# Kernel tuning notes

Measured on AMD Instinct MI355X. Metric: run time of the kernel, lower is better.

The kernel has to match this reference:

```python
import jax, jax.numpy as jnp
import numpy as np

B, M, N, DQ, H = 4, 4096, 4096, 256, 64

def setup_inputs() -> dict:
    key = jax.random.key(0)
    k1, k2, k3, k4 = jax.random.split(key, 4)
    x = jax.random.normal(k1, (B, M, DQ), dtype=jnp.float32)
    cond = jax.random.normal(k2, (B, N, DQ), dtype=jnp.float32)
    Wq = jax.random.normal(k3, (DQ, H), dtype=jnp.float32) * (1.0 / np.sqrt(DQ))
    Wkv = jax.random.normal(k4, (DQ, 2 * H), dtype=jnp.float32) * (1.0 / np.sqrt(DQ))
    return {"x": x, "cond": cond, "Wq": Wq, "Wkv": Wkv}

def reference(x, cond, Wq, Wkv):
    h = Wq.shape[1]
    q = jnp.einsum('bmi,ih->bmh', x, Wq)          # [B,M,H]
    kv = jnp.einsum('bni,ih->bnh', cond, Wkv)     # [B,N,2H]
    k, v = jnp.split(kv, 2, axis=-1)              # each [B,N,H]
    qk = jnp.einsum('bmd,bnd->bmn', q, k) / jnp.sqrt(jnp.asarray(h, q.dtype))
    attn = jax.nn.softmax(qk, axis=-1)            # [B,M,N]
    out = jnp.einsum('bmn,bnd->bmd', attn, v)     # [B,M,H]
    return out
```

## Files before the change

kernel.cpp:

```cpp
#include <hip/hip_runtime.h>
#include <hip/hip_bf16.h>
#include <cstdint>


#define BB 4
#define MM 4096
#define NN 4096
#define DQm 256
#define DH 64
#define NSP 4
#define QSCALE 0.18033688011112042f

typedef _Float16 half8 __attribute__((ext_vector_type(8)));
typedef _Float16 half4 __attribute__((ext_vector_type(4)));
typedef float floatx16 __attribute__((ext_vector_type(16)));

static __device__ __forceinline__ unsigned pkrtz(float a, float b) {
    union { __fp16 h __attribute__((ext_vector_type(2))); unsigned u; } cv;
    cv.h = __builtin_amdgcn_cvt_pkrtz(a, b);
    return cv.u;
}

__global__ __launch_bounds__(256) void wtrans_kernel(const float* __restrict__ Wq,
                                                     const float* __restrict__ Wkv,
                                                     _Float16* __restrict__ wt) {
    int cout = blockIdx.x;
    int t = threadIdx.x;
    float v = (cout < 64) ? Wq[t * 64 + cout] * QSCALE : Wkv[t * 128 + (cout - 64)];
    _Float16 hi = (_Float16)v;
    _Float16 lo = (_Float16)(v - (float)hi);
    wt[cout * DQm + t] = hi;
    wt[192 * DQm + cout * DQm + t] = lo;
}

__global__ __launch_bounds__(256) void qproj_kernel(const float* __restrict__ x,
                                                    const _Float16* __restrict__ wt,
                                                    _Float16* __restrict__ q_h) {
    __shared__ __align__(16) _Float16 xh[64][264];
    __shared__ __align__(16) _Float16 xl[64][264];
    const int t = threadIdx.x;
    const long row0 = (long)blockIdx.x * 64;
    const float4* xg = (const float4*)(x + row0 * DQm);
#pragma unroll
    for (int it = 0; it < 16; ++it) {
        int fid = t + it * 256;
        int row = fid >> 6, c4 = fid & 63;
        float4 v = xg[fid];
        half4 hh = {(_Float16)v.x, (_Float16)v.y, (_Float16)v.z, (_Float16)v.w};
        half4 hl = {(_Float16)(v.x - (float)hh[0]), (_Float16)(v.y - (float)hh[1]),
                    (_Float16)(v.z - (float)hh[2]), (_Float16)(v.w - (float)hh[3])};
        *(half4*)(&xh[row][c4 * 4]) = hh;
        *(half4*)(&xl[row][c4 * 4]) = hl;
    }
    __syncthreads();
    const int lane = t & 63, w = t >> 6, c = lane & 31, h = lane >> 5;
    const int rt = w & 1, ct = w >> 1;
    const _Float16* wlo = wt + 192 * DQm;
    floatx16 a1, a2, a3;
#pragma unroll
    for (int i = 0; i < 16; ++i) { a1[i] = 0.f; a2[i] = 0.f; a3[i] = 0.f; }
#pragma unroll
    for (int kt = 0; kt < 16; ++kt) {
        half8 ah = *(const half8*)(&xh[rt * 32 + c][kt * 16 + h * 8]);
        half8 al = *(const half8*)(&xl[rt * 32 + c][kt * 16 + h * 8]);
        half8 bh = *(const half8*)(wt  + (long)(ct * 32 + c) * DQm + kt * 16 + h * 8);
        half8 bl = *(const half8*)(wlo + (long)(ct * 32 + c) * DQm + kt * 16 + h * 8);
        a1 = __builtin_amdgcn_mfma_f32_32x32x16_f16(ah, bh, a1, 0, 0, 0);
        a2 = __builtin_amdgcn_mfma_f32_32x32x16_f16(ah, bl, a2, 0, 0, 0);
        a3 = __builtin_amdgcn_mfma_f32_32x32x16_f16(al, bh, a3, 0, 0, 0);
    }
#pragma unroll
    for (int r = 0; r < 16; ++r) {
        int m = (r & 3) + 8 * (r >> 2) + 4 * h;
        q_h[(row0 + rt * 32 + m) * DH + ct * 32 + c] = (_Float16)(a1[r] + a2[r] + a3[r]);
    }
}

__global__ __launch_bounds__(256) void kvproj_kernel(const float* __restrict__ cond,
                                                     const _Float16* __restrict__ wt,
                                                     _Float16* __restrict__ k_h,
                                                     _Float16* __restrict__ vt_h) {
    __shared__ __align__(16) _Float16 xh[64][264];
    __shared__ __align__(16) _Float16 xl[64][264];
    const int t = threadIdx.x;
    const long row0 = (long)blockIdx.x * 64;
    const float4* xg = (const float4*)(cond + row0 * DQm);
#pragma unroll
    for (int it = 0; it < 16; ++it) {
        int fid = t + it * 256;
        int row = fid >> 6, c4 = fid & 63;
        float4 v = xg[fid];
        half4 hh = {(_Float16)v.x, (_Float16)v.y, (_Float16)v.z, (_Float16)v.w};
        half4 hl = {(_Float16)(v.x - (float)hh[0]), (_Float16)(v.y - (float)hh[1]),
                    (_Float16)(v.z - (float)hh[2]), (_Float16)(v.w - (float)hh[3])};
        *(half4*)(&xh[row][c4 * 4]) = hh;
        *(half4*)(&xl[row][c4 * 4]) = hl;
    }
    __syncthreads();
    const int lane = t & 63, w = t >> 6, c = lane & 31, h = lane >> 5;
    const int rt = w & 1, ctp = w >> 1;
    const _Float16* wlo = wt + 192 * DQm;
    floatx16 a1[2], a2[2], a3[2];
#pragma unroll
    for (int i = 0; i < 16; ++i) {
        a1[0][i] = 0.f; a2[0][i] = 0.f; a3[0][i] = 0.f;
        a1[1][i] = 0.f; a2[1][i] = 0.f; a3[1][i] = 0.f;
    }
#pragma unroll
    for (int kt = 0; kt < 16; ++kt) {
        half8 ah = *(const half8*)(&xh[rt * 32 + c][kt * 16 + h * 8]);
        half8 al = *(const half8*)(&xl[rt * 32 + c][kt * 16 + h * 8]);
#pragma unroll
        for (int i = 0; i < 2; ++i) {
            long wrow = 64 + (ctp * 2 + i) * 32 + c;
            half8 bh = *(const half8*)(wt  + wrow * DQm + kt * 16 + h * 8);
            half8 bl = *(const half8*)(wlo + wrow * DQm + kt * 16 + h * 8);
            a1[i] = __builtin_amdgcn_mfma_f32_32x32x16_f16(ah, bh, a1[i], 0, 0, 0);
            a2[i] = __builtin_amdgcn_mfma_f32_32x32x16_f16(ah, bl, a2[i], 0, 0, 0);
            a3[i] = __builtin_amdgcn_mfma_f32_32x32x16_f16(al, bh, a3[i], 0, 0, 0);
        }
    }
#pragma unroll
    for (int i = 0; i < 2; ++i) {
        int cout = (ctp * 2 + i) * 32 + c;
        if (cout < 64) {
#pragma unroll
            for (int r = 0; r < 16; ++r) {
                int m = (r & 3) + 8 * (r >> 2) + 4 * h;
                k_h[(row0 + rt * 32 + m) * DH + cout] =
                    (_Float16)(a1[i][r] + a2[i][r] + a3[i][r]);
            }
        } else {
            int d = cout - 64;
            long bb = row0 >> 12;
#pragma unroll
            for (int s2 = 0; s2 < 4; ++s2) {
                long n = row0 + rt * 32 + 8 * s2 + 4 * h;
                half4 hv;
#pragma unroll
                for (int j = 0; j < 4; ++j)
                    hv[j] = (_Float16)(a1[i][s2 * 4 + j] + a2[i][s2 * 4 + j] +
                                       a3[i][s2 * 4 + j]);
                *(half4*)(vt_h + (bb * DH + d) * NN + (n & 4095)) = hv;
            }
        }
    }
}

__global__ __launch_bounds__(256, 2) void fa_kernel(const _Float16* __restrict__ q_h,
                                                    const _Float16* __restrict__ k_h,
                                                    const _Float16* __restrict__ vt_h,
                                                    float* __restrict__ Opart,
                                                    float2* __restrict__ ml) {
    __shared__ __align__(16) _Float16 k_lds[64][72];
    __shared__ __align__(16) _Float16 vt_lds[64][72];

    const int t = threadIdx.x;
    const int w = t >> 6;
    const int lane = t & 63;
    const int c = lane & 31;
    const int h = lane >> 5;

    const int bid = blockIdx.x;
    const int sp = bid >> 7;
    const int b  = (bid >> 5) & 3;
    const int mt = bid & 31;
    const int mbase = mt * 128 + w * 32;
    const long qrow = (long)b * MM + mbase + c;

    half8 qf[4];
#pragma unroll
    for (int kt = 0; kt < 4; ++kt)
        qf[kt] = *(const half8*)(q_h + qrow * DH + kt * 16 + h * 8);

    floatx16 Oc0, Oc1;
#pragma unroll
    for (int i = 0; i < 16; ++i) { Oc0[i] = 0.f; Oc1[i] = 0.f; }
    float m_run = -INFINITY, l_run = 0.f;

#pragma unroll 1
    for (int nt = sp * 16; nt < sp * 16 + 16; ++nt) {
        const int n0 = nt * 64;
        __syncthreads();
        {
            const uint4* kg = (const uint4*)(k_h + ((long)b * NN + n0) * DH);
#pragma unroll
            for (int it = 0; it < 2; ++it) {
                int cid = t + it * 256;
                int r = cid >> 3, q = cid & 7;
                *(uint4*)(&k_lds[r][q * 8]) = kg[cid];
                *(uint4*)(&vt_lds[r][q * 8]) =
                    *(const uint4*)(vt_h + ((long)b * DH + r) * NN + n0 + q * 8);
            }
        }
        __syncthreads();

        floatx16 Sc[2];
#pragma unroll
        for (int a = 0; a < 2; ++a) {
            floatx16 acc;
#pragma unroll
            for (int i = 0; i < 16; ++i) acc[i] = 0.f;
#pragma unroll
            for (int kt = 0; kt < 4; ++kt) {
                half8 af = *(const half8*)(&k_lds[a * 32 + c][kt * 16 + h * 8]);
                acc = __builtin_amdgcn_mfma_f32_32x32x16_f16(af, qf[kt], acc, 0, 0, 0);
            }
            Sc[a] = acc;
        }

        float tmax = -INFINITY;
#pragma unroll
        for (int a = 0; a < 2; ++a)
#pragma unroll
            for (int r = 0; r < 16; ++r) tmax = fmaxf(tmax, Sc[a][r]);
        tmax = fmaxf(tmax, __shfl_xor(tmax, 32, 64));
        float m_new = fmaxf(m_run, tmax);
        float alpha = exp2f(m_run - m_new);
        float tsum = 0.f;
#pragma unroll
        for (int a = 0; a < 2; ++a)
#pragma unroll
            for (int r = 0; r < 16; ++r) {
                float p = exp2f(Sc[a][r] - m_new);
                Sc[a][r] = p;
                tsum += p;
            }
        tsum += __shfl_xor(tsum, 32, 64);
        l_run = l_run * alpha + tsum;
        m_run = m_new;
#pragma unroll
        for (int i = 0; i < 16; ++i) { Oc0[i] *= alpha; Oc1[i] *= alpha; }

#pragma unroll
        for (int a = 0; a < 2; ++a) {
            uint2 pk0 = {pkrtz(Sc[a][0],  Sc[a][1]),  pkrtz(Sc[a][2],  Sc[a][3])};
            uint2 pk1 = {pkrtz(Sc[a][4],  Sc[a][5]),  pkrtz(Sc[a][6],  Sc[a][7])};
            uint2 pk2 = {pkrtz(Sc[a][8],  Sc[a][9]),  pkrtz(Sc[a][10], Sc[a][11])};
            uint2 pk3 = {pkrtz(Sc[a][12], Sc[a][13]), pkrtz(Sc[a][14], Sc[a][15])};
            uint2 s0, s1, ex0, ex1;
            s0.x = h ? pk0.x : pk1.x;  s0.y = h ? pk0.y : pk1.y;
            s1.x = h ? pk2.x : pk3.x;  s1.y = h ? pk2.y : pk3.y;
            ex0.x = __shfl_xor((int)s0.x, 32, 64);
            ex0.y = __shfl_xor((int)s0.y, 32, 64);
            ex1.x = __shfl_xor((int)s1.x, 32, 64);
            ex1.y = __shfl_xor((int)s1.y, 32, 64);
            union { uint4 u; half8 f; } f0, f1;
            f0.u.x = h ? ex0.x : pk0.x;  f0.u.y = h ? ex0.y : pk0.y;
            f0.u.z = h ? pk1.x : ex0.x;  f0.u.w = h ? pk1.y : ex0.y;
            f1.u.x = h ? ex1.x : pk2.x;  f1.u.y = h ? ex1.y : pk2.y;
            f1.u.z = h ? pk3.x : ex1.x;  f1.u.w = h ? pk3.y : ex1.y;
#pragma unroll
            for (int bq = 0; bq < 2; ++bq) {
                int kt = 2 * a + bq;
                half8 pf = bq ? f1.f : f0.f;
                half8 vf0 = *(const half8*)(&vt_lds[c][kt * 16 + h * 8]);
                half8 vf1 = *(const half8*)(&vt_lds[32 + c][kt * 16 + h * 8]);
                Oc0 = __builtin_amdgcn_mfma_f32_32x32x16_f16(vf0, pf, Oc0, 0, 0, 0);
                Oc1 = __builtin_amdgcn_mfma_f32_32x32x16_f16(vf1, pf, Oc1, 0, 0, 0);
            }
        }
    }

    const long obase = ((long)sp * BB * MM + (long)b * MM + mbase + c) * DH;
#pragma unroll
    for (int dt = 0; dt < 2; ++dt) {
        const floatx16& O = dt ? Oc1 : Oc0;
#pragma unroll
        for (int s2 = 0; s2 < 4; ++s2) {
            float4 v;
            v.x = O[s2 * 4 + 0]; v.y = O[s2 * 4 + 1];
            v.z = O[s2 * 4 + 2]; v.w = O[s2 * 4 + 3];
            *(float4*)(Opart + obase + dt * 32 + s2 * 8 + h * 4) = v;
        }
    }
    if (h == 0)
        ml[((long)sp * BB + b) * MM + mbase + c] = make_float2(m_run, l_run);
}

__global__ __launch_bounds__(256) void merge_kernel(const float* __restrict__ Opart,
                                                    const float2* __restrict__ ml,
                                                    float* __restrict__ out) {
    const long gid = (long)blockIdx.x * 256 + threadIdx.x;
    const long row = gid >> 6;
    float2 p[NSP];
    float mmax = -INFINITY;
#pragma unroll
    for (int i = 0; i < NSP; ++i) {
        p[i] = ml[(long)i * BB * MM + row];
        mmax = fmaxf(mmax, p[i].x);
    }
    float denom = 0.f, o = 0.f;
#pragma unroll
    for (int i = 0; i < NSP; ++i) {
        float ai = exp2f(p[i].x - mmax);
        denom += ai * p[i].y;
        o += ai * Opart[(long)i * BB * MM * DH + gid];
    }
    out[gid] = o / denom;
}

extern "C" void kernel_launch(void* const* d_in, const int* in_sizes, int n_in,
                              void* d_out, int out_size, void* d_ws, size_t ws_size,
                              hipStream_t stream) {
    const float* x    = (const float*)d_in[0];
    const float* cond = (const float*)d_in[1];
    const float* Wq   = (const float*)d_in[2];
    const float* Wkv  = (const float*)d_in[3];
    float* out = (float*)d_out;

    char* ws = (char*)d_ws;
    _Float16* wt   = (_Float16*)(ws);
    _Float16* q_h  = (_Float16*)(ws + 196608);
    _Float16* k_h  = (_Float16*)(ws + 196608 + 2097152);
    _Float16* vt_h = (_Float16*)(ws + 196608 + 2 * 2097152);
    float*    Op   = (float*)(ws + 196608 + 3 * 2097152);
    float2*   mlp  = (float2*)(ws + 196608 + 3 * 2097152 + (size_t)NSP * 4194304);

    wtrans_kernel<<<192, 256, 0, stream>>>(Wq, Wkv, wt);
    qproj_kernel<<<BB * MM / 64, 256, 0, stream>>>(x, wt, q_h);
    kvproj_kernel<<<BB * NN / 64, 256, 0, stream>>>(cond, wt, k_h, vt_h);
    fa_kernel<<<NSP * BB * 32, 256, 0, stream>>>(q_h, k_h, vt_h, Op, mlp);
    merge_kernel<<<BB * MM * DH / 256, 256, 0, stream>>>(Op, mlp, out);
}
```

Before: 138.2 us.

## Merge projection kernels, double split-K, lazy softmax rescale, permlane32 swap

Fuses the Q and KV projection kernels into one launch so both run concurrently. Doubles the number of key-dimension splits in the attention kernel and raises the launch-bounds occupancy hint from 2 to 4 blocks per CU, giving more blocks and shorter loops. The online softmax now rescales the running max and accumulators only when some lane's new max exceeds the old one by more than 8 (log2 domain). P fragments are exchanged with permlane32_swap instead of shuffles. The trade-offs are more partial outputs for the merge kernel to combine, tighter register limits, and a bounded range for unnormalised exponentials.

Measured after the change: 134.9 us. 2.4% less time.

```diff
diff --git a/kernel.cpp b/kernel.cpp
--- a/kernel.cpp
+++ b/kernel.cpp
@@ -8,7 +8,8 @@
 #define NN 4096
 #define DQm 256
 #define DH 64
-#define NSP 4
+#define NSP 8
+#define NITER (NN / 64 / NSP)
 #define QSCALE 0.18033688011112042f
 
 typedef _Float16 half8 __attribute__((ext_vector_type(8)));
@@ -33,14 +34,19 @@
     wt[192 * DQm + cout * DQm + t] = lo;
 }
 
-__global__ __launch_bounds__(256) void qproj_kernel(const float* __restrict__ x,
-                                                    const _Float16* __restrict__ wt,
-                                                    _Float16* __restrict__ q_h) {
+__global__ __launch_bounds__(256) void proj_kernel(const float* __restrict__ x,
+                                                   const float* __restrict__ cond,
+                                                   const _Float16* __restrict__ wt,
+                                                   _Float16* __restrict__ q_h,
+                                                   _Float16* __restrict__ k_h,
+                                                   _Float16* __restrict__ vt_h) {
     __shared__ __align__(16) _Float16 xh[64][264];
     __shared__ __align__(16) _Float16 xl[64][264];
     const int t = threadIdx.x;
-    const long row0 = (long)blockIdx.x * 64;
-    const float4* xg = (const float4*)(x + row0 * DQm);
+    const bool isq = blockIdx.x < (BB * MM / 64);
+    const int blk = isq ? blockIdx.x : blockIdx.x - BB * MM / 64;
+    const long row0 = (long)blk * 64;
+    const float4* xg = (const float4*)((isq ? x : cond) + row0 * DQm);
 #pragma unroll
     for (int it = 0; it < 16; ++it) {
         int fid = t + it * 256;
@@ -54,100 +60,79 @@
     }
     __syncthreads();
     const int lane = t & 63, w = t >> 6, c = lane & 31, h = lane >> 5;
-    const int rt = w & 1, ct = w >> 1;
     const _Float16* wlo = wt + 192 * DQm;
-    floatx16 a1, a2, a3;
-#pragma unroll
-    for (int i = 0; i < 16; ++i) { a1[i] = 0.f; a2[i] = 0.f; a3[i] = 0.f; }
-#pragma unroll
-    for (int kt = 0; kt < 16; ++kt) {
-        half8 ah = *(const half8*)(&xh[rt * 32 + c][kt * 16 + h * 8]);
-        half8 al = *(const half8*)(&xl[rt * 32 + c][kt * 16 + h * 8]);
-        half8 bh = *(const half8*)(wt  + (long)(ct * 32 + c) * DQm + kt * 16 + h * 8);
-        half8 bl = *(const half8*)(wlo + (long)(ct * 32 + c) * DQm + kt * 16 + h * 8);
-        a1 = __builtin_amdgcn_mfma_f32_32x32x16_f16(ah, bh, a1, 0, 0, 0);
-        a2 = __builtin_amdgcn_mfma_f32_32x32x16_f16(ah, bl, a2, 0, 0, 0);
-        a3 = __builtin_amdgcn_mfma_f32_32x32x16_f16(al, bh, a3, 0, 0, 0);
-    }
-#pragma unroll
-    for (int r = 0; r < 16; ++r) {
-        int m = (r & 3) + 8 * (r >> 2) + 4 * h;
-        q_h[(row0 + rt * 32 + m) * DH + ct * 32 + c] = (_Float16)(a1[r] + a2[r] + a3[r]);
-    }
-}
-
-__global__ __launch_bounds__(256) void kvproj_kernel(const float* __restrict__ cond,
-                                                     const _Float16* __restrict__ wt,
-                                                     _Float16* __restrict__ k_h,
-                                                     _Float16* __restrict__ vt_h) {
-    __shared__ __align__(16) _Float16 xh[64][264];
-    __shared__ __align__(16) _Float16 xl[64][264];
-    const int t = threadIdx.x;
-    const long row0 = (long)blockIdx.x * 64;
-    const float4* xg = (const float4*)(cond + row0 * DQm);
-#pragma unroll
-    for (int it = 0; it < 16; ++it) {
-        int fid = t + it * 256;
-        int row = fid >> 6, c4 = fid & 63;
-        float4 v = xg[fid];
-        half4 hh = {(_Float16)v.x, (_Float16)v.y, (_Float16)v.z, (_Float16)v.w};
-        half4 hl = {(_Float16)(v.x - (float)hh[0]), (_Float16)(v.y - (float)hh[1]),
-                    (_Float16)(v.z - (float)hh[2]), (_Float16)(v.w - (float)hh[3])};
-        *(half4*)(&xh[row][c4 * 4]) = hh;
-        *(half4*)(&xl[row][c4 * 4]) = hl;
-    }
-    __syncthreads();
-    const int lane = t & 63, w = t >> 6, c = lane & 31, h = lane >> 5;
-    const int rt = w & 1, ctp = w >> 1;
-    const _Float16* wlo = wt + 192 * DQm;
-    floatx16 a1[2], a2[2], a3[2];
-#pragma unroll
-    for (int i = 0; i < 16; ++i) {
-        a1[0][i] = 0.f; a2[0][i] = 0.f; a3[0][i] = 0.f;
-        a1[1][i] = 0.f; a2[1][i] = 0.f; a3[1][i] = 0.f;
-    }
-#pragma unroll
-    for (int kt = 0; kt < 16; ++kt) {
-        half8 ah = *(const half8*)(&xh[rt * 32 + c][kt * 16 + h * 8]);
-        half8 al = *(const half8*)(&xl[rt * 32 + c][kt * 16 + h * 8]);
+
+    if (isq) {
+        const int rt = w & 1, ct = w >> 1;
+        floatx16 a1, a2, a3;
+#pragma unroll
+        for (int i = 0; i < 16; ++i) { a1[i] = 0.f; a2[i] = 0.f; a3[i] = 0.f; }
+#pragma unroll
+        for (int kt = 0; kt < 16; ++kt) {
+            half8 ah = *(const half8*)(&xh[rt * 32 + c][kt * 16 + h * 8]);
+            half8 al = *(const half8*)(&xl[rt * 32 + c][kt * 16 + h * 8]);
+            half8 bh = *(const half8*)(wt  + (long)(ct * 32 + c) * DQm + kt * 16 + h * 8);
+            half8 bl = *(const half8*)(wlo + (long)(ct * 32 + c) * DQm + kt * 16 + h * 8);
+            a1 = __builtin_amdgcn_mfma_f32_32x32x16_f16(ah, bh, a1, 0, 0, 0);
+            a2 = __builtin_amdgcn_mfma_f32_32x32x16_f16(ah, bl, a2, 0, 0, 0);
+            a3 = __builtin_amdgcn_mfma_f32_32x32x16_f16(al, bh, a3, 0, 0, 0);
+        }
+#pragma unroll
+        for (int r = 0; r < 16; ++r) {
+            int m = (r & 3) + 8 * (r >> 2) + 4 * h;
+            q_h[(row0 + rt * 32 + m) * DH + ct * 32 + c] = (_Float16)(a1[r] + a2[r] + a3[r]);
+        }
+    } else {
+        const int rt = w & 1, ctp = w >> 1;
+        floatx16 a1[2], a2[2], a3[2];
+#pragma unroll
+        for (int i = 0; i < 16; ++i) {
+            a1[0][i] = 0.f; a2[0][i] = 0.f; a3[0][i] = 0.f;
+            a1[1][i] = 0.f; a2[1][i] = 0.f; a3[1][i] = 0.f;
+        }
+#pragma unroll
+        for (int kt = 0; kt < 16; ++kt) {
+            half8 ah = *(const half8*)(&xh[rt * 32 + c][kt * 16 + h * 8]);
+            half8 al = *(const half8*)(&xl[rt * 32 + c][kt * 16 + h * 8]);
+#pragma unroll
+            for (int i = 0; i < 2; ++i) {
+                long wrow = 64 + (ctp * 2 + i) * 32 + c;
+                half8 bh = *(const half8*)(wt  + wrow * DQm + kt * 16 + h * 8);
+                half8 bl = *(const half8*)(wlo + wrow * DQm + kt * 16 + h * 8);
+                a1[i] = __builtin_amdgcn_mfma_f32_32x32x16_f16(ah, bh, a1[i], 0, 0, 0);
+                a2[i] = __builtin_amdgcn_mfma_f32_32x32x16_f16(ah, bl, a2[i], 0, 0, 0);
+                a3[i] = __builtin_amdgcn_mfma_f32_32x32x16_f16(al, bh, a3[i], 0, 0, 0);
+            }
+        }
 #pragma unroll
         for (int i = 0; i < 2; ++i) {
-            long wrow = 64 + (ctp * 2 + i) * 32 + c;
-            half8 bh = *(const half8*)(wt  + wrow * DQm + kt * 16 + h * 8);
-            half8 bl = *(const half8*)(wlo + wrow * DQm + kt * 16 + h * 8);
-            a1[i] = __builtin_amdgcn_mfma_f32_32x32x16_f16(ah, bh, a1[i], 0, 0, 0);
-            a2[i] = __builtin_amdgcn_mfma_f32_32x32x16_f16(ah, bl, a2[i], 0, 0, 0);
-            a3[i] = __builtin_amdgcn_mfma_f32_32x32x16_f16(al, bh, a3[i], 0, 0, 0);
-        }
-    }
-#pragma unroll
-    for (int i = 0; i < 2; ++i) {
-        int cout = (ctp * 2 + i) * 32 + c;
-        if (cout < 64) {
-#pragma unroll
-            for (int r = 0; r < 16; ++r) {
-                int m = (r & 3) + 8 * (r >> 2) + 4 * h;
-                k_h[(row0 + rt * 32 + m) * DH + cout] =
-                    (_Float16)(a1[i][r] + a2[i][r] + a3[i][r]);
-            }
-        } else {
-            int d = cout - 64;
-            long bb = row0 >> 12;
-#pragma unroll
-            for (int s2 = 0; s2 < 4; ++s2) {
-                long n = row0 + rt * 32 + 8 * s2 + 4 * h;
-                half4 hv;
-#pragma unroll
-                for (int j = 0; j < 4; ++j)
-                    hv[j] = (_Float16)(a1[i][s2 * 4 + j] + a2[i][s2 * 4 + j] +
-                                       a3[i][s2 * 4 + j]);
-                *(half4*)(vt_h + (bb * DH + d) * NN + (n & 4095)) = hv;
-            }
-        }
-    }
-}
-
-__global__ __launch_bounds__(256, 2) void fa_kernel(const _Float16* __restrict__ q_h,
+            int cout = (ctp * 2 + i) * 32 + c;
+            if (cout < 64) {
+#pragma unroll
+                for (int r = 0; r < 16; ++r) {
+                    int m = (r & 3) + 8 * (r >> 2) + 4 * h;
+                    k_h[(row0 + rt * 32 + m) * DH + cout] =
+                        (_Float16)(a1[i][r] + a2[i][r] + a3[i][r]);
+                }
+            } else {
+                int d = cout - 64;
+                long bb = row0 >> 12;
+#pragma unroll
+                for (int s2 = 0; s2 < 4; ++s2) {
+                    long n = row0 + rt * 32 + 8 * s2 + 4 * h;
+                    half4 hv;
+#pragma unroll
+                    for (int j = 0; j < 4; ++j)
+                        hv[j] = (_Float16)(a1[i][s2 * 4 + j] + a2[i][s2 * 4 + j] +
+                                           a3[i][s2 * 4 + j]);
+                    *(half4*)(vt_h + (bb * DH + d) * NN + (n & 4095)) = hv;
+                }
+            }
+        }
+    }
+}
+
+__global__ __launch_bounds__(256, 4) void fa_kernel(const _Float16* __restrict__ q_h,
                                                     const _Float16* __restrict__ k_h,
                                                     const _Float16* __restrict__ vt_h,
                                                     float* __restrict__ Opart,
@@ -179,7 +164,7 @@
     float m_run = -INFINITY, l_run = 0.f;
 
 #pragma unroll 1
-    for (int nt = sp * 16; nt < sp * 16 + 16; ++nt) {
+    for (int nt = sp * NITER; nt < sp * NITER + NITER; ++nt) {
         const int n0 = nt * 64;
         __syncthreads();
         {
@@ -215,22 +200,25 @@
 #pragma unroll
             for (int r = 0; r < 16; ++r) tmax = fmaxf(tmax, Sc[a][r]);
         tmax = fmaxf(tmax, __shfl_xor(tmax, 32, 64));
-        float m_new = fmaxf(m_run, tmax);
-        float alpha = exp2f(m_run - m_new);
+        if (__any(tmax > m_run + 8.0f)) {
+            float m_new = fmaxf(m_run, tmax);
+            float alpha = exp2f(m_run - m_new);
+            l_run *= alpha;
+#pragma unroll
+            for (int i = 0; i < 16; ++i) { Oc0[i] *= alpha; Oc1[i] *= alpha; }
+            m_run = m_new;
+        }
         float tsum = 0.f;
 #pragma unroll
         for (int a = 0; a < 2; ++a)
 #pragma unroll
             for (int r = 0; r < 16; ++r) {
-                float p = exp2f(Sc[a][r] - m_new);
+                float p = exp2f(Sc[a][r] - m_run);
                 Sc[a][r] = p;
                 tsum += p;
             }
         tsum += __shfl_xor(tsum, 32, 64);
-        l_run = l_run * alpha + tsum;
-        m_run = m_new;
-#pragma unroll
-        for (int i = 0; i < 16; ++i) { Oc0[i] *= alpha; Oc1[i] *= alpha; }
+        l_run += tsum;
 
 #pragma unroll
         for (int a = 0; a < 2; ++a) {
@@ -238,18 +226,33 @@
             uint2 pk1 = {pkrtz(Sc[a][4],  Sc[a][5]),  pkrtz(Sc[a][6],  Sc[a][7])};
             uint2 pk2 = {pkrtz(Sc[a][8],  Sc[a][9]),  pkrtz(Sc[a][10], Sc[a][11])};
             uint2 pk3 = {pkrtz(Sc[a][12], Sc[a][13]), pkrtz(Sc[a][14], Sc[a][15])};
-            uint2 s0, s1, ex0, ex1;
-            s0.x = h ? pk0.x : pk1.x;  s0.y = h ? pk0.y : pk1.y;
-            s1.x = h ? pk2.x : pk3.x;  s1.y = h ? pk2.y : pk3.y;
-            ex0.x = __shfl_xor((int)s0.x, 32, 64);
-            ex0.y = __shfl_xor((int)s0.y, 32, 64);
-            ex1.x = __shfl_xor((int)s1.x, 32, 64);
-            ex1.y = __shfl_xor((int)s1.y, 32, 64);
             union { uint4 u; half8 f; } f0, f1;
-            f0.u.x = h ? ex0.x : pk0.x;  f0.u.y = h ? ex0.y : pk0.y;
-            f0.u.z = h ? pk1.x : ex0.x;  f0.u.w = h ? pk1.y : ex0.y;
-            f1.u.x = h ? ex1.x : pk2.x;  f1.u.y = h ? ex1.y : pk2.y;
-            f1.u.z = h ? pk3.x : ex1.x;  f1.u.w = h ? pk3.y : ex1.y;
+#if __has_builtin(__builtin_amdgcn_permlane32_swap)
+            {
+                auto r0 = __builtin_amdgcn_permlane32_swap(pk0.x, pk1.x, false, false);
+                auto r1 = __builtin_amdgcn_permlane32_swap(pk0.y, pk1.y, false, false);
+                auto r2 = __builtin_amdgcn_permlane32_swap(pk2.x, pk3.x, false, false);
+                auto r3 = __builtin_amdgcn_permlane32_swap(pk2.y, pk3.y, false, false);
+                f0.u.x = r0[0]; f0.u.z = r0[1];
+                f0.u.y = r1[0]; f0.u.w = r1[1];
+                f1.u.x = r2[0]; f1.u.z = r2[1];
+                f1.u.y = r3[0]; f1.u.w = r3[1];
+            }
+#else
+            {
+                uint2 s0, s1, ex0, ex1;
+                s0.x = h ? pk0.x : pk1.x;  s0.y = h ? pk0.y : pk1.y;
+                s1.x = h ? pk2.x : pk3.x;  s1.y = h ? pk2.y : pk3.y;
+                ex0.x = __shfl_xor((int)s0.x, 32, 64);
+                ex0.y = __shfl_xor((int)s0.y, 32, 64);
+                ex1.x = __shfl_xor((int)s1.x, 32, 64);
+                ex1.y = __shfl_xor((int)s1.y, 32, 64);
+                f0.u.x = h ? ex0.x : pk0.x;  f0.u.y = h ? ex0.y : pk0.y;
+                f0.u.z = h ? pk1.x : ex0.x;  f0.u.w = h ? pk1.y : ex0.y;
+                f1.u.x = h ? ex1.x : pk2.x;  f1.u.y = h ? ex1.y : pk2.y;
+                f1.u.z = h ? pk3.x : ex1.x;  f1.u.w = h ? pk3.y : ex1.y;
+            }
+#endif
 #pragma unroll
             for (int bq = 0; bq < 2; ++bq) {
                 int kt = 2 * a + bq;
@@ -318,8 +321,7 @@
     float2*   mlp  = (float2*)(ws + 196608 + 3 * 2097152 + (size_t)NSP * 4194304);
 
     wtrans_kernel<<<192, 256, 0, stream>>>(Wq, Wkv, wt);
-    qproj_kernel<<<BB * MM / 64, 256, 0, stream>>>(x, wt, q_h);
-    kvproj_kernel<<<BB * NN / 64, 256, 0, stream>>>(cond, wt, k_h, vt_h);
+    proj_kernel<<<BB * (MM + NN) / 64, 256, 0, stream>>>(x, cond, wt, q_h, k_h, vt_h);
     fa_kernel<<<NSP * BB * 32, 256, 0, stream>>>(q_h, k_h, vt_h, Op, mlp);
     merge_kernel<<<BB * MM * DH / 256, 256, 0, stream>>>(Op, mlp, out);
 }
```
